# Kernel optimization log

Hardware: AMD Instinct MI355X
Metric: run time of the kernel (lower is better)

Reference implementation:

```python
import jax, jax.numpy as jnp
import numpy as np
import math

B, T, S, D, H = 2, 1024, 1024, 1024, 16
DH = D // H


def setup_inputs() -> dict:
    key = jax.random.key(0)
    ks = jax.random.split(key, 13)
    scale = 1.0 / math.sqrt(D)
    inp = {
        "q": jax.random.normal(ks[0], (B, T, D), jnp.float32),
        "k": jax.random.normal(ks[1], (B, S, D), jnp.float32),
        "v": jax.random.normal(ks[2], (B, S, D), jnp.float32),
        # causal mask: True means masked
        "attn_mask": jnp.broadcast_to(
            jnp.triu(jnp.ones((T, S), jnp.bool_), k=1)[None, None], (B, 1, T, S)
        ),
        "attn_bias": jax.random.normal(ks[3], (B, H, T, S), jnp.float32),
        "Wq": jax.random.normal(ks[4], (D, D), jnp.float32) * scale,
        "bq": jnp.zeros((D,), jnp.float32),
        "Wk": jax.random.normal(ks[5], (D, D), jnp.float32) * scale,
        "bk": jnp.zeros((D,), jnp.float32),
        "Wv": jax.random.normal(ks[6], (D, D), jnp.float32) * scale,
        "bv": jnp.zeros((D,), jnp.float32),
        "Wo": jax.random.normal(ks[7], (D, D), jnp.float32) * scale,
        "bo": jnp.zeros((D,), jnp.float32),
        "bias_scale": jnp.asarray(0.5, jnp.float32),
    }
    return inp


def reference(q, k, v, attn_mask, attn_bias, Wq, bq, Wk, bk, Wv, bv, Wo, bo, bias_scale):
    # projections (torch Linear convention: x @ W.T + b), split heads
    qh = (q @ Wq.T + bq).reshape(B, T, H, DH)   # (B,T,H,DH)
    kh = (k @ Wk.T + bk).reshape(B, S, H, DH)
    vh = (v @ Wv.T + bv).reshape(B, S, H, DH)

    scores = jnp.einsum("bthd,bshd->bhts", qh, kh) / math.sqrt(DH)  # (B,H,T,S)
    scores = jnp.clip(scores, -80.0, 80.0)
    scores = jnp.where(attn_mask, -jnp.inf, scores)  # mask broadcasts over H
    attn = jax.nn.softmax(scores, axis=-1)

    # post-softmax multiplicative bias + renormalize
    scale = 1.0 + bias_scale * jnp.tanh(attn_bias)
    attn = attn * jnp.maximum(scale, 1e-9)
    attn = attn / (jnp.sum(attn, axis=-1, keepdims=True) + 1e-9)

    # dropout p=0.0 (eval) -> identity
    out = jnp.einsum("bhts,bshd->bthd", attn, vh).reshape(B, T, D)
    out = out @ Wo.T + bo
    return out, attn
```

## Files before the change

### kernel.cpp

```cpp
#include <hip/hip_runtime.h>
#include <hip/hip_bf16.h>
#include <math.h>

#define BB 2
#define TT 1024
#define SS 1024
#define DD 1024
#define HH 16
#define DH 64

typedef __attribute__((ext_vector_type(8))) short bf16x8;
typedef __attribute__((ext_vector_type(4))) float f32x4;
typedef unsigned short ushort_t;

#define AS3(p) ((__attribute__((address_space(3))) unsigned int*)(p))
#define AS1(p) ((const __attribute__((address_space(1))) unsigned int*)(p))

__device__ __forceinline__ unsigned short f2b(float f) {
    union { float f; unsigned u; } x; x.f = f;
    unsigned r = x.u + 0x7FFFu + ((x.u >> 16) & 1u);
    return (unsigned short)(r >> 16);
}

__global__ __launch_bounds__(256) void cvt3_kernel(
    const float* __restrict__ a, const float* __restrict__ b, const float* __restrict__ c,
    ushort_t* __restrict__ oa, ushort_t* __restrict__ ob, ushort_t* __restrict__ oc)
{
    const float* src = (blockIdx.y == 0) ? a : (blockIdx.y == 1) ? b : c;
    ushort_t* dst    = (blockIdx.y == 0) ? oa : (blockIdx.y == 1) ? ob : oc;
    size_t i = ((size_t)blockIdx.x * 256 + threadIdx.x) * 8;
    float4 v0 = *(const float4*)&src[i];
    float4 v1 = *(const float4*)&src[i + 4];
    uint4 o;
    o.x = f2b(v0.x) | ((unsigned)f2b(v0.y) << 16);
    o.y = f2b(v0.z) | ((unsigned)f2b(v0.w) << 16);
    o.z = f2b(v1.x) | ((unsigned)f2b(v1.y) << 16);
    o.w = f2b(v1.z) | ((unsigned)f2b(v1.w) << 16);
    *(uint4*)&dst[i] = o;
}

__global__ __launch_bounds__(256) void cvt4_kernel(
    const float* __restrict__ a, const float* __restrict__ b,
    const float* __restrict__ c, const float* __restrict__ d,
    ushort_t* __restrict__ oa, ushort_t* __restrict__ ob,
    ushort_t* __restrict__ oc, ushort_t* __restrict__ od)
{
    const float* src = (blockIdx.y == 0) ? a : (blockIdx.y == 1) ? b : (blockIdx.y == 2) ? c : d;
    ushort_t* dst    = (blockIdx.y == 0) ? oa : (blockIdx.y == 1) ? ob : (blockIdx.y == 2) ? oc : od;
    size_t i = ((size_t)blockIdx.x * 256 + threadIdx.x) * 8;
    float4 v0 = *(const float4*)&src[i];
    float4 v1 = *(const float4*)&src[i + 4];
    uint4 o;
    o.x = f2b(v0.x) | ((unsigned)f2b(v0.y) << 16);
    o.y = f2b(v0.z) | ((unsigned)f2b(v0.w) << 16);
    o.z = f2b(v1.x) | ((unsigned)f2b(v1.y) << 16);
    o.w = f2b(v1.z) | ((unsigned)f2b(v1.w) << 16);
    *(uint4*)&dst[i] = o;
}

__device__ __forceinline__ void gemm128_mainloop(
    const ushort_t* __restrict__ A,
    const ushort_t* __restrict__ Bw,
    int K, ushort_t* Asm, ushort_t* Bsm, f32x4 acc[4][4])
{
    const int tid = threadIdx.x;
    const int wave = tid >> 6, lane = tid & 63;
    const int sr = lane >> 2;
    const int gc = (lane & 3) ^ ((lane >> 3) & 3);
    const int l15 = lane & 15, q = lane >> 4;
    const int mblk = (wave >> 1) * 64, nblk = (wave & 1) * 64;

    for (int k0 = 0; k0 < K; k0 += 32) {
        #pragma unroll
        for (int o = 0; o < 2; o++) {
            int r0 = (wave * 2 + o) * 16;
            __builtin_amdgcn_global_load_lds(AS1(A + (size_t)(r0 + sr) * K + k0 + gc * 8),
                                             AS3(Asm + r0 * 32), 16, 0, 0);
            __builtin_amdgcn_global_load_lds(AS1(Bw + (size_t)(r0 + sr) * K + k0 + gc * 8),
                                             AS3(Bsm + r0 * 32), 16, 0, 0);
        }
        __syncthreads();

        bf16x8 av[4], bv[4];
        #pragma unroll
        for (int mi = 0; mi < 4; mi++) {
            int r = mblk + mi * 16 + l15;
            av[mi] = *(const bf16x8*)&Asm[r * 32 + (q ^ ((r >> 1) & 3)) * 8];
        }
        #pragma unroll
        for (int ni = 0; ni < 4; ni++) {
            int r = nblk + ni * 16 + l15;
            bv[ni] = *(const bf16x8*)&Bsm[r * 32 + (q ^ ((r >> 1) & 3)) * 8];
        }
        #pragma unroll
        for (int mi = 0; mi < 4; mi++)
            #pragma unroll
            for (int ni = 0; ni < 4; ni++)
                acc[mi][ni] = __builtin_amdgcn_mfma_f32_16x16x32_bf16(av[mi], bv[ni], acc[mi][ni], 0, 0, 0);
        __syncthreads();
    }
}

__global__ __launch_bounds__(256) void proj_gemm(
    const ushort_t* __restrict__ qb, const ushort_t* __restrict__ kb, const ushort_t* __restrict__ vb,
    const ushort_t* __restrict__ Wqb, const ushort_t* __restrict__ Wkb, const ushort_t* __restrict__ Wvb,
    const float* __restrict__ bq, const float* __restrict__ bk, const float* __restrict__ bv,
    ushort_t* __restrict__ qh, ushort_t* __restrict__ kh, ushort_t* __restrict__ vh)
{
    __shared__ ushort_t Asm[128 * 32];
    __shared__ ushort_t Bsm[128 * 32];
    const int z = blockIdx.z;
    const ushort_t* A = (z == 0) ? qb : (z == 1) ? kb : vb;
    const ushort_t* W = (z == 0) ? Wqb : (z == 1) ? Wkb : Wvb;
    const float* bias = (z == 0) ? bq : (z == 1) ? bk : bv;
    ushort_t* Y = (z == 0) ? qh : (z == 1) ? kh : vh;

    const int bm = blockIdx.y * 128, bn = blockIdx.x * 128;
    f32x4 acc[4][4];
    #pragma unroll
    for (int i = 0; i < 4; i++)
        #pragma unroll
        for (int j = 0; j < 4; j++) acc[i][j] = (f32x4)(0.f);

    gemm128_mainloop(A + (size_t)bm * DD, W + (size_t)bn * DD, DD, Asm, Bsm, acc);

    const int lane = threadIdx.x & 63, wave = threadIdx.x >> 6;
    const int mblk = (wave >> 1) * 64, nblk = (wave & 1) * 64;
    const int l15 = lane & 15, q = lane >> 4;
    #pragma unroll
    for (int mi = 0; mi < 4; mi++) {
        #pragma unroll
        for (int ni = 0; ni < 4; ni++) {
            int col = bn + nblk + ni * 16 + l15;
            float bcol = bias[col];
            #pragma unroll
            for (int r = 0; r < 4; r++) {
                int row = bm + mblk + mi * 16 + q * 4 + r;
                Y[(size_t)row * DD + col] = f2b(acc[mi][ni][r] + bcol);
            }
        }
    }
}

__global__ __launch_bounds__(256) void oproj_gemm(
    const ushort_t* __restrict__ A, const ushort_t* __restrict__ W,
    const float* __restrict__ bias, float* __restrict__ Y)
{
    __shared__ ushort_t Asm[128 * 32];
    __shared__ ushort_t Bsm[128 * 32];
    const int bm = blockIdx.y * 128, bn = blockIdx.x * 128;
    f32x4 acc[4][4];
    #pragma unroll
    for (int i = 0; i < 4; i++)
        #pragma unroll
        for (int j = 0; j < 4; j++) acc[i][j] = (f32x4)(0.f);

    gemm128_mainloop(A + (size_t)bm * DD, W + (size_t)bn * DD, DD, Asm, Bsm, acc);

    const int lane = threadIdx.x & 63, wave = threadIdx.x >> 6;
    const int mblk = (wave >> 1) * 64, nblk = (wave & 1) * 64;
    const int l15 = lane & 15, q = lane >> 4;
    #pragma unroll
    for (int mi = 0; mi < 4; mi++) {
        #pragma unroll
        for (int ni = 0; ni < 4; ni++) {
            int col = bn + nblk + ni * 16 + l15;
            float bcol = bias[col];
            #pragma unroll
            for (int r = 0; r < 4; r++) {
                int row = bm + mblk + mi * 16 + q * 4 + r;
                Y[(size_t)row * DD + col] = acc[mi][ni][r] + bcol;
            }
        }
    }
}

__global__ __launch_bounds__(256) void transpose_v(
    const ushort_t* __restrict__ vh, ushort_t* __restrict__ vT)
{
    __shared__ ushort_t Ls[64][72];
    const int s0 = blockIdx.x * 64;
    const int bh = blockIdx.y;
    const int b = bh >> 4, h = bh & 15;
    const int tid = threadIdx.x;
    const int r = tid >> 2, c16 = (tid & 3) * 16;

    const ushort_t* src = &vh[((size_t)(b * SS + s0 + r) * HH + h) * DH + c16];
    uint4 u0 = *(const uint4*)src;
    uint4 u1 = *(const uint4*)(src + 8);
    ushort_t tmp[16];
    *(uint4*)&tmp[0] = u0; *(uint4*)&tmp[8] = u1;
    #pragma unroll
    for (int j = 0; j < 16; j++) Ls[c16 + j][r] = tmp[j];
    __syncthreads();

    const int dh = r;
    uint4 w0 = *(const uint4*)&Ls[dh][c16];
    uint4 w1 = *(const uint4*)&Ls[dh][c16 + 8];
    ushort_t* dst = &vT[((size_t)bh * DH + dh) * SS + s0 + c16];
    *(uint4*)dst = w0;
    *(uint4*)(dst + 8) = w1;
}

__global__ __launch_bounds__(256) void scores_mfma(
    const ushort_t* __restrict__ qh, const ushort_t* __restrict__ kh,
    float* __restrict__ attn)
{
    __shared__ ushort_t Qs[128 * 64];
    __shared__ ushort_t Ks[128 * 64];

    int idx = blockIdx.x, ti = 0;
    while (idx >= ti + 1) { idx -= ti + 1; ti++; }
    const int si = idx;
    const int bh = blockIdx.y;
    const int b = bh >> 4, h = bh & 15;
    const int t0 = ti * 128, s0 = si * 128;

    const int tid = threadIdx.x;
    const int wave = tid >> 6, lane = tid & 63;
    const int sr8 = lane >> 3;
    const int gc8 = (lane & 7) ^ sr8;

    #pragma unroll
    for (int o = 0; o < 4; o++) {
        int r0 = (wave * 4 + o) * 8;
        int r = r0 + sr8;
        __builtin_amdgcn_global_load_lds(
            AS1(qh + ((size_t)(b * TT + t0 + r) * HH + h) * DH + gc8 * 8),
            AS3(Qs + r0 * 64), 16, 0, 0);
        __builtin_amdgcn_global_load_lds(
            AS1(kh + ((size_t)(b * SS + s0 + r) * HH + h) * DH + gc8 * 8),
            AS3(Ks + r0 * 64), 16, 0, 0);
    }
    __syncthreads();

    const int l15 = lane & 15, q = lane >> 4;
    const int tblk = (wave >> 1) * 64, sblk = (wave & 1) * 64;
    f32x4 acc[4][4];
    #pragma unroll
    for (int i = 0; i < 4; i++)
        #pragma unroll
        for (int j = 0; j < 4; j++) acc[i][j] = (f32x4)(0.f);

    #pragma unroll
    for (int ks = 0; ks < 2; ks++) {
        bf16x8 av[4], bv[4];
        #pragma unroll
        for (int mi = 0; mi < 4; mi++) {
            int r = tblk + mi * 16 + l15;
            av[mi] = *(const bf16x8*)&Qs[r * 64 + ((ks * 4 + q) ^ (r & 7)) * 8];
        }
        #pragma unroll
        for (int ni = 0; ni < 4; ni++) {
            int r = sblk + ni * 16 + l15;
            bv[ni] = *(const bf16x8*)&Ks[r * 64 + ((ks * 4 + q) ^ (r & 7)) * 8];
        }
        #pragma unroll
        for (int mi = 0; mi < 4; mi++)
            #pragma unroll
            for (int ni = 0; ni < 4; ni++)
                acc[mi][ni] = __builtin_amdgcn_mfma_f32_16x16x32_bf16(av[mi], bv[ni], acc[mi][ni], 0, 0, 0);
    }

    #pragma unroll
    for (int mi = 0; mi < 4; mi++) {
        #pragma unroll
        for (int ni = 0; ni < 4; ni++) {
            int scol = s0 + sblk + ni * 16 + l15;
            #pragma unroll
            for (int r = 0; r < 4; r++) {
                int t = t0 + tblk + mi * 16 + q * 4 + r;
                float v = acc[mi][ni][r] * 0.125f;
                v = fminf(fmaxf(v, -80.f), 80.f);
                attn[((size_t)bh * TT + t) * SS + scol] = v;
            }
        }
    }
}

__global__ __launch_bounds__(256) void softmax_bias_kernel(
    const float* __restrict__ attn_bias, const float* __restrict__ bias_scale_p,
    float* __restrict__ attn)
{
    const int bid = blockIdx.x;
    const int t = bid & (TT - 1);
    const int tid = threadIdx.x;
    const int s0 = tid * 4;

    float* row = attn + (size_t)bid * SS;
    const float* brow = attn_bias + (size_t)bid * SS;

    __shared__ float red[256];

    float v0 = -INFINITY, v1 = -INFINITY, v2 = -INFINITY, v3 = -INFINITY;
    if (s0 <= t) {
        float4 rv = *(const float4*)&row[s0];
        v0 = rv.x;
        v1 = (s0 + 1 <= t) ? rv.y : -INFINITY;
        v2 = (s0 + 2 <= t) ? rv.z : -INFINITY;
        v3 = (s0 + 3 <= t) ? rv.w : -INFINITY;
    }
    float lmax = fmaxf(fmaxf(v0, v1), fmaxf(v2, v3));
    red[tid] = lmax;
    __syncthreads();
    for (int off = 128; off > 0; off >>= 1) {
        if (tid < off) red[tid] = fmaxf(red[tid], red[tid + off]);
        __syncthreads();
    }
    const float m = red[0];
    __syncthreads();

    float p0 = (v0 > -INFINITY) ? __expf(v0 - m) : 0.f;
    float p1 = (v1 > -INFINITY) ? __expf(v1 - m) : 0.f;
    float p2 = (v2 > -INFINITY) ? __expf(v2 - m) : 0.f;
    float p3 = (v3 > -INFINITY) ? __expf(v3 - m) : 0.f;
    red[tid] = p0 + p1 + p2 + p3;
    __syncthreads();
    for (int off = 128; off > 0; off >>= 1) {
        if (tid < off) red[tid] += red[tid + off];
        __syncthreads();
    }
    const float inv = 1.f / red[0];
    __syncthreads();

    const float bscale = bias_scale_p[0];
    float w0 = 0.f, w1 = 0.f, w2 = 0.f, w3 = 0.f;
    if (s0 <= t) {
        float4 bv = *(const float4*)&brow[s0];
        float e0 = __expf(-2.f * fabsf(bv.x));
        float e1 = __expf(-2.f * fabsf(bv.y));
        float e2 = __expf(-2.f * fabsf(bv.z));
        float e3 = __expf(-2.f * fabsf(bv.w));
        float t0 = copysignf((1.f - e0) / (1.f + e0), bv.x);
        float t1 = copysignf((1.f - e1) / (1.f + e1), bv.y);
        float t2 = copysignf((1.f - e2) / (1.f + e2), bv.z);
        float t3 = copysignf((1.f - e3) / (1.f + e3), bv.w);
        w0 = p0 * inv * fmaxf(1.f + bscale * t0, 1e-9f);
        w1 = p1 * inv * fmaxf(1.f + bscale * t1, 1e-9f);
        w2 = p2 * inv * fmaxf(1.f + bscale * t2, 1e-9f);
        w3 = p3 * inv * fmaxf(1.f + bscale * t3, 1e-9f);
    }
    red[tid] = w0 + w1 + w2 + w3;
    __syncthreads();
    for (int off = 128; off > 0; off >>= 1) {
        if (tid < off) red[tid] += red[tid + off];
        __syncthreads();
    }
    const float inv2 = 1.f / (red[0] + 1e-9f);

    float4 o;
    o.x = w0 * inv2; o.y = w1 * inv2; o.z = w2 * inv2; o.w = w3 * inv2;
    *(float4*)&row[s0] = o;
}

__global__ __launch_bounds__(256) void av_mfma(
    const float* __restrict__ attn, const ushort_t* __restrict__ vT,
    ushort_t* __restrict__ ao)
{
    __shared__ ushort_t Asm[64 * 32];
    __shared__ ushort_t Vsm[64 * 32];

    const int tb = blockIdx.x;
    const int bh = blockIdx.y;
    const int b = bh >> 4, h = bh & 15;
    const int t0 = tb * 64;
    const int nsteps = (tb + 1) * 2;

    const int tid = threadIdx.x;
    const int wave = tid >> 6, lane = tid & 63;
    const int ar = tid >> 2, aq = tid & 3;
    const int aslot = aq ^ ((ar >> 1) & 3);
    const int vsr = lane >> 2;
    const int vgc = (lane & 3) ^ ((lane >> 3) & 3);
    const int l15 = lane & 15, q = lane >> 4;

    f32x4 acc[4];
    #pragma unroll
    for (int i = 0; i < 4; i++) acc[i] = (f32x4)(0.f);

    for (int st = 0; st < nsteps; st++) {
        const int s0 = st * 32;
        {
            const float* src = &attn[((size_t)bh * TT + t0 + ar) * SS + s0 + aq * 8];
            float4 u0 = *(const float4*)src;
            float4 u1 = *(const float4*)(src + 4);
            uint4 o;
            o.x = f2b(u0.x) | ((unsigned)f2b(u0.y) << 16);
            o.y = f2b(u0.z) | ((unsigned)f2b(u0.w) << 16);
            o.z = f2b(u1.x) | ((unsigned)f2b(u1.y) << 16);
            o.w = f2b(u1.z) | ((unsigned)f2b(u1.w) << 16);
            *(uint4*)&Asm[ar * 32 + aslot * 8] = o;
        }
        {
            int r0 = wave * 16;
            __builtin_amdgcn_global_load_lds(
                AS1(vT + ((size_t)bh * DH + r0 + vsr) * SS + s0 + vgc * 8),
                AS3(Vsm + r0 * 32), 16, 0, 0);
        }
        __syncthreads();

        bf16x8 a0, bv[4];
        {
            int r = wave * 16 + l15;
            a0 = *(const bf16x8*)&Asm[r * 32 + (q ^ ((r >> 1) & 3)) * 8];
        }
        #pragma unroll
        for (int ni = 0; ni < 4; ni++) {
            int r = ni * 16 + l15;
            bv[ni] = *(const bf16x8*)&Vsm[r * 32 + (q ^ ((r >> 1) & 3)) * 8];
        }
        #pragma unroll
        for (int ni = 0; ni < 4; ni++)
            acc[ni] = __builtin_amdgcn_mfma_f32_16x16x32_bf16(a0, bv[ni], acc[ni], 0, 0, 0);
        __syncthreads();
    }

    #pragma unroll
    for (int ni = 0; ni < 4; ni++) {
        int dh = ni * 16 + l15;
        #pragma unroll
        for (int r = 0; r < 4; r++) {
            int t = t0 + wave * 16 + q * 4 + r;
            ao[(size_t)(b * TT + t) * DD + h * DH + dh] = f2b(acc[ni][r]);
        }
    }
}

extern "C" void kernel_launch(void* const* d_in, const int* in_sizes, int n_in,
                              void* d_out, int out_size, void* d_ws, size_t ws_size,
                              hipStream_t stream)
{
    const float* q   = (const float*)d_in[0];
    const float* k   = (const float*)d_in[1];
    const float* v   = (const float*)d_in[2];
    const float* attn_bias = (const float*)d_in[4];
    const float* Wq = (const float*)d_in[5];
    const float* bq = (const float*)d_in[6];
    const float* Wk = (const float*)d_in[7];
    const float* bk = (const float*)d_in[8];
    const float* Wv = (const float*)d_in[9];
    const float* bv = (const float*)d_in[10];
    const float* Wo = (const float*)d_in[11];
    const float* bo = (const float*)d_in[12];
    const float* bscale = (const float*)d_in[13];

    char* base = (char*)d_ws;
    ushort_t* qb  = (ushort_t*)(base + (0ull << 20));
    ushort_t* kb  = (ushort_t*)(base + (4ull << 20));
    ushort_t* vb  = (ushort_t*)(base + (8ull << 20));
    ushort_t* Wqb = (ushort_t*)(base + (12ull << 20));
    ushort_t* Wkb = (ushort_t*)(base + (14ull << 20));
    ushort_t* Wvb = (ushort_t*)(base + (16ull << 20));
    ushort_t* Wob = (ushort_t*)(base + (18ull << 20));
    ushort_t* qhb = (ushort_t*)(base + (20ull << 20));
    ushort_t* khb = (ushort_t*)(base + (24ull << 20));
    ushort_t* vhb = (ushort_t*)(base + (28ull << 20));
    ushort_t* vT  = qb;
    ushort_t* aob = kb;

    float* out  = (float*)d_out;
    float* attn = out + (size_t)BB * TT * DD;

    cvt3_kernel<<<dim3(1024, 3), 256, 0, stream>>>(q, k, v, qb, kb, vb);
    cvt4_kernel<<<dim3(512, 4), 256, 0, stream>>>(Wq, Wk, Wv, Wo, Wqb, Wkb, Wvb, Wob);
    proj_gemm<<<dim3(8, 16, 3), 256, 0, stream>>>(qb, kb, vb, Wqb, Wkb, Wvb,
                                                  bq, bk, bv, qhb, khb, vhb);
    transpose_v<<<dim3(16, 32), 256, 0, stream>>>(vhb, vT);
    scores_mfma<<<dim3(36, 32), 256, 0, stream>>>(qhb, khb, attn);
    softmax_bias_kernel<<<dim3(BB * HH * TT), 256, 0, stream>>>(attn_bias, bscale, attn);
    av_mfma<<<dim3(16, 32), 256, 0, stream>>>(attn, vT, aob);
    oproj_gemm<<<dim3(8, 16), 256, 0, stream>>>(aob, Wob, bo, out);
}
```

Measured before the change: 390.1 us.

## Fuse scores, softmax, bias renormalization and AV into one flash-style attention kernel

Replaces the separate scores, softmax+bias and AV kernels with a single two-pass kernel per 64-row query tile. The first pass computes the row max over causal key blocks. The second pass recomputes scores, applies the exp and tanh-bias scale, writes unnormalized bf16 weights to a scratch buffer, and accumulates P·V with MFMA. A final sweep normalizes and writes the fp32 attn output, and the two float conversion kernels are merged into one launch. This removes the full fp32 attention round trips through global memory. In exchange it recomputes QK^T, keeps an extra bf16 scratch pass, and rounds the attn output through bf16. It also drops the 1e-9 term in the final renormalisation.

```diff
diff --git a/kernel.cpp b/kernel.cpp
--- a/kernel.cpp
+++ b/kernel.cpp
@@ -22,12 +22,27 @@
     return (unsigned short)(r >> 16);
 }
 
-__global__ __launch_bounds__(256) void cvt3_kernel(
-    const float* __restrict__ a, const float* __restrict__ b, const float* __restrict__ c,
-    ushort_t* __restrict__ oa, ushort_t* __restrict__ ob, ushort_t* __restrict__ oc)
-{
-    const float* src = (blockIdx.y == 0) ? a : (blockIdx.y == 1) ? b : c;
-    ushort_t* dst    = (blockIdx.y == 0) ? oa : (blockIdx.y == 1) ? ob : oc;
+__global__ __launch_bounds__(256) void cvt_all(
+    const float* __restrict__ q, const float* __restrict__ k, const float* __restrict__ v,
+    const float* __restrict__ Wq, const float* __restrict__ Wk,
+    const float* __restrict__ Wv, const float* __restrict__ Wo,
+    ushort_t* __restrict__ qb, ushort_t* __restrict__ kb, ushort_t* __restrict__ vb,
+    ushort_t* __restrict__ Wqb, ushort_t* __restrict__ Wkb,
+    ushort_t* __restrict__ Wvb, ushort_t* __restrict__ Wob)
+{
+    const int z = blockIdx.y;
+    if (z >= 3 && blockIdx.x >= 512) return;
+    const float* src;
+    ushort_t* dst;
+    switch (z) {
+        case 0: src = q;  dst = qb;  break;
+        case 1: src = k;  dst = kb;  break;
+        case 2: src = v;  dst = vb;  break;
+        case 3: src = Wq; dst = Wqb; break;
+        case 4: src = Wk; dst = Wkb; break;
+        case 5: src = Wv; dst = Wvb; break;
+        default: src = Wo; dst = Wob; break;
+    }
     size_t i = ((size_t)blockIdx.x * 256 + threadIdx.x) * 8;
     float4 v0 = *(const float4*)&src[i];
     float4 v1 = *(const float4*)&src[i + 4];
@@ -39,28 +54,8 @@
     *(uint4*)&dst[i] = o;
 }
 
-__global__ __launch_bounds__(256) void cvt4_kernel(
-    const float* __restrict__ a, const float* __restrict__ b,
-    const float* __restrict__ c, const float* __restrict__ d,
-    ushort_t* __restrict__ oa, ushort_t* __restrict__ ob,
-    ushort_t* __restrict__ oc, ushort_t* __restrict__ od)
-{
-    const float* src = (blockIdx.y == 0) ? a : (blockIdx.y == 1) ? b : (blockIdx.y == 2) ? c : d;
-    ushort_t* dst    = (blockIdx.y == 0) ? oa : (blockIdx.y == 1) ? ob : (blockIdx.y == 2) ? oc : od;
-    size_t i = ((size_t)blockIdx.x * 256 + threadIdx.x) * 8;
-    float4 v0 = *(const float4*)&src[i];
-    float4 v1 = *(const float4*)&src[i + 4];
-    uint4 o;
-    o.x = f2b(v0.x) | ((unsigned)f2b(v0.y) << 16);
-    o.y = f2b(v0.z) | ((unsigned)f2b(v0.w) << 16);
-    o.z = f2b(v1.x) | ((unsigned)f2b(v1.y) << 16);
-    o.w = f2b(v1.z) | ((unsigned)f2b(v1.w) << 16);
-    *(uint4*)&dst[i] = o;
-}
-
 __device__ __forceinline__ void gemm128_mainloop(
-    const ushort_t* __restrict__ A,
-    const ushort_t* __restrict__ Bw,
+    const ushort_t* __restrict__ A, const ushort_t* __restrict__ Bw,
     int K, ushort_t* Asm, ushort_t* Bsm, f32x4 acc[4][4])
 {
     const int tid = threadIdx.x;
@@ -185,7 +180,7 @@
     const int tid = threadIdx.x;
     const int r = tid >> 2, c16 = (tid & 3) * 16;
 
-    const ushort_t* src = &vh[((size_t)(b * SS + s0 + r) * HH + h) * DH + c16];
+    const ushort_t* src = &vh[((size_t)(b * SS + s0 + r)) * DD + h * DH + c16];
     uint4 u0 = *(const uint4*)src;
     uint4 u1 = *(const uint4*)(src + 8);
     ushort_t tmp[16];
@@ -202,228 +197,269 @@
     *(uint4*)(dst + 8) = w1;
 }
 
-__global__ __launch_bounds__(256) void scores_mfma(
+#define SCORE_MFMA(sacc)                                                        \
+  do {                                                                          \
+    _Pragma("unroll")                                                           \
+    for (int ks = 0; ks < 2; ks++) {                                            \
+      bf16x8 af[2], bfv[4];                                                     \
+      _Pragma("unroll")                                                         \
+      for (int mi = 0; mi < 2; mi++) {                                          \
+        int row_ = mq * 32 + mi * 16 + l15;                                     \
+        af[mi] = *(const bf16x8*)&Qs[row_ * 64 + ((ks * 4 + q) ^ (row_ & 7)) * 8]; \
+      }                                                                         \
+      _Pragma("unroll")                                                         \
+      for (int ni = 0; ni < 4; ni++) {                                          \
+        int srw_ = nq * 64 + ni * 16 + l15;                                     \
+        bfv[ni] = *(const bf16x8*)&Ks[srw_ * 64 + ((ks * 4 + q) ^ (srw_ & 7)) * 8]; \
+      }                                                                         \
+      _Pragma("unroll")                                                         \
+      for (int mi = 0; mi < 2; mi++)                                            \
+        _Pragma("unroll")                                                       \
+        for (int ni = 0; ni < 4; ni++)                                          \
+          sacc[mi][ni] = __builtin_amdgcn_mfma_f32_16x16x32_bf16(af[mi], bfv[ni], sacc[mi][ni], 0, 0, 0); \
+    }                                                                           \
+  } while (0)
+
+#define STAGE_K(s0_)                                                            \
+  do {                                                                          \
+    _Pragma("unroll")                                                           \
+    for (int o = 0; o < 4; o++) {                                               \
+      int slot = o * 256 + tid;                                                 \
+      int row_ = slot >> 3, cs_ = slot & 7, c_ = cs_ ^ (row_ & 7);              \
+      __builtin_amdgcn_global_load_lds(                                         \
+          AS1(kh + (size_t)(b * SS + (s0_) + row_) * DD + h * DH + c_ * 8),     \
+          AS3(Ks + (o * 256 + wave * 64) * 8), 16, 0, 0);                       \
+    }                                                                           \
+  } while (0)
+
+#define STAGE_V(s0_)                                                            \
+  do {                                                                          \
+    _Pragma("unroll")                                                           \
+    for (int o = 0; o < 4; o++) {                                               \
+      int slot = o * 256 + tid;                                                 \
+      int row_ = slot >> 4, cs_ = slot & 15, c_ = cs_ ^ (row_ & 15);            \
+      __builtin_amdgcn_global_load_lds(                                         \
+          AS1(vT + ((size_t)bh * DH + row_) * SS + (s0_) + c_ * 8),             \
+          AS3(Vs + (o * 256 + wave * 64) * 8), 16, 0, 0);                       \
+    }                                                                           \
+  } while (0)
+
+__global__ __launch_bounds__(256, 2) void flash_attn(
     const ushort_t* __restrict__ qh, const ushort_t* __restrict__ kh,
+    const ushort_t* __restrict__ vT, const float* __restrict__ attn_bias,
+    const float* __restrict__ bscale_p,
+    ushort_t* __restrict__ wbuf, ushort_t* __restrict__ ao,
     float* __restrict__ attn)
 {
-    __shared__ ushort_t Qs[128 * 64];
-    __shared__ ushort_t Ks[128 * 64];
-
-    int idx = blockIdx.x, ti = 0;
-    while (idx >= ti + 1) { idx -= ti + 1; ti++; }
-    const int si = idx;
+    __shared__ alignas(16) ushort_t Qs[64 * 64];
+    __shared__ alignas(16) ushort_t Ks[128 * 64];
+    __shared__ alignas(16) ushort_t Vs[64 * 128];
+    __shared__ alignas(16) ushort_t Ws[64 * 136];
+    __shared__ float rmax_p[2][64];
+    __shared__ float rsum_p[2][64];
+    __shared__ float rstat[64];
+
+    const int xs = blockIdx.x;
+    const int ti = (xs & 1) ? (15 - (xs >> 1)) : (xs >> 1);
     const int bh = blockIdx.y;
     const int b = bh >> 4, h = bh & 15;
-    const int t0 = ti * 128, s0 = si * 128;
+    const int t0 = ti * 64;
+    const int nst = (ti >> 1) + 1;
 
     const int tid = threadIdx.x;
     const int wave = tid >> 6, lane = tid & 63;
-    const int sr8 = lane >> 3;
-    const int gc8 = (lane & 7) ^ sr8;
-
-    #pragma unroll
-    for (int o = 0; o < 4; o++) {
-        int r0 = (wave * 4 + o) * 8;
-        int r = r0 + sr8;
+    const int l15 = lane & 15, q = lane >> 4;
+    const int mq = wave & 1, nq = wave >> 1;
+
+    #pragma unroll
+    for (int o = 0; o < 2; o++) {
+        int slot = o * 256 + tid;
+        int row_ = slot >> 3, cs_ = slot & 7, c_ = cs_ ^ (row_ & 7);
         __builtin_amdgcn_global_load_lds(
-            AS1(qh + ((size_t)(b * TT + t0 + r) * HH + h) * DH + gc8 * 8),
-            AS3(Qs + r0 * 64), 16, 0, 0);
-        __builtin_amdgcn_global_load_lds(
-            AS1(kh + ((size_t)(b * SS + s0 + r) * HH + h) * DH + gc8 * 8),
-            AS3(Ks + r0 * 64), 16, 0, 0);
+            AS1(qh + (size_t)(b * TT + t0 + row_) * DD + h * DH + c_ * 8),
+            AS3(Qs + (o * 256 + wave * 64) * 8), 16, 0, 0);
+    }
+
+    float rm[2][4];
+    #pragma unroll
+    for (int mi = 0; mi < 2; mi++)
+        #pragma unroll
+        for (int r = 0; r < 4; r++) rm[mi][r] = -INFINITY;
+
+    for (int si = 0; si < nst; si++) {
+        const int s0 = si * 128;
+        STAGE_K(s0);
+        __syncthreads();
+        f32x4 sacc[2][4];
+        #pragma unroll
+        for (int mi = 0; mi < 2; mi++)
+            #pragma unroll
+            for (int ni = 0; ni < 4; ni++) sacc[mi][ni] = (f32x4)(0.f);
+        SCORE_MFMA(sacc);
+        #pragma unroll
+        for (int mi = 0; mi < 2; mi++)
+            #pragma unroll
+            for (int ni = 0; ni < 4; ni++) {
+                int s = s0 + nq * 64 + ni * 16 + l15;
+                #pragma unroll
+                for (int r = 0; r < 4; r++) {
+                    int t = t0 + mq * 32 + mi * 16 + q * 4 + r;
+                    if (s <= t) {
+                        float v = fminf(fmaxf(sacc[mi][ni][r] * 0.125f, -80.f), 80.f);
+                        rm[mi][r] = fmaxf(rm[mi][r], v);
+                    }
+                }
+            }
+        __syncthreads();
+    }
+    #pragma unroll
+    for (int mi = 0; mi < 2; mi++)
+        #pragma unroll
+        for (int r = 0; r < 4; r++) {
+            float v = rm[mi][r];
+            v = fmaxf(v, __shfl_xor(v, 1));
+            v = fmaxf(v, __shfl_xor(v, 2));
+            v = fmaxf(v, __shfl_xor(v, 4));
+            v = fmaxf(v, __shfl_xor(v, 8));
+            rm[mi][r] = v;
+        }
+    if (l15 == 0) {
+        #pragma unroll
+        for (int mi = 0; mi < 2; mi++)
+            #pragma unroll
+            for (int r = 0; r < 4; r++)
+                rmax_p[nq][mq * 32 + mi * 16 + q * 4 + r] = rm[mi][r];
     }
     __syncthreads();
-
-    const int l15 = lane & 15, q = lane >> 4;
-    const int tblk = (wave >> 1) * 64, sblk = (wave & 1) * 64;
-    f32x4 acc[4][4];
-    #pragma unroll
-    for (int i = 0; i < 4; i++)
-        #pragma unroll
-        for (int j = 0; j < 4; j++) acc[i][j] = (f32x4)(0.f);
-
-    #pragma unroll
-    for (int ks = 0; ks < 2; ks++) {
-        bf16x8 av[4], bv[4];
-        #pragma unroll
-        for (int mi = 0; mi < 4; mi++) {
-            int r = tblk + mi * 16 + l15;
-            av[mi] = *(const bf16x8*)&Qs[r * 64 + ((ks * 4 + q) ^ (r & 7)) * 8];
-        }
-        #pragma unroll
-        for (int ni = 0; ni < 4; ni++) {
-            int r = sblk + ni * 16 + l15;
-            bv[ni] = *(const bf16x8*)&Ks[r * 64 + ((ks * 4 + q) ^ (r & 7)) * 8];
-        }
-        #pragma unroll
-        for (int mi = 0; mi < 4; mi++)
-            #pragma unroll
-            for (int ni = 0; ni < 4; ni++)
-                acc[mi][ni] = __builtin_amdgcn_mfma_f32_16x16x32_bf16(av[mi], bv[ni], acc[mi][ni], 0, 0, 0);
-    }
-
-    #pragma unroll
-    for (int mi = 0; mi < 4; mi++) {
-        #pragma unroll
-        for (int ni = 0; ni < 4; ni++) {
-            int scol = s0 + sblk + ni * 16 + l15;
+    if (tid < 64) rstat[tid] = fmaxf(rmax_p[0][tid], rmax_p[1][tid]);
+    __syncthreads();
+
+    float rs[2][4] = {};
+    f32x4 oacc[2][2];
+    #pragma unroll
+    for (int mi = 0; mi < 2; mi++)
+        #pragma unroll
+        for (int ni = 0; ni < 2; ni++) oacc[mi][ni] = (f32x4)(0.f);
+    const float bs = bscale_p[0];
+
+    for (int si = 0; si < nst; si++) {
+        const int s0 = si * 128;
+        STAGE_K(s0);
+        STAGE_V(s0);
+        __syncthreads();
+        f32x4 sacc[2][4];
+        #pragma unroll
+        for (int mi = 0; mi < 2; mi++)
+            #pragma unroll
+            for (int ni = 0; ni < 4; ni++) sacc[mi][ni] = (f32x4)(0.f);
+        SCORE_MFMA(sacc);
+
+        #pragma unroll
+        for (int mi = 0; mi < 2; mi++)
+            #pragma unroll
+            for (int ni = 0; ni < 4; ni++) {
+                int sc_ = nq * 64 + ni * 16 + l15;
+                int s = s0 + sc_;
+                #pragma unroll
+                for (int r = 0; r < 4; r++) {
+                    int trow = mq * 32 + mi * 16 + q * 4 + r;
+                    int t = t0 + trow;
+                    float w = 0.f;
+                    if (s <= t) {
+                        float v = fminf(fmaxf(sacc[mi][ni][r] * 0.125f, -80.f), 80.f);
+                        float x = attn_bias[((size_t)bh * TT + t) * SS + s];
+                        float e = __expf(-2.f * fabsf(x));
+                        float th = copysignf((1.f - e) / (1.f + e), x);
+                        float scl = fmaxf(1.f + bs * th, 1e-9f);
+                        w = __expf(v - rstat[trow]) * scl;
+                        rs[mi][r] += w;
+                    }
+                    Ws[trow * 136 + sc_] = f2b(w);
+                }
+            }
+        __syncthreads();
+
+        #pragma unroll
+        for (int o = 0; o < 4; o++) {
+            int idx = o * 256 + tid;
+            int row_ = idx >> 4, c_ = idx & 15;
+            uint4 u = *(const uint4*)&Ws[row_ * 136 + c_ * 8];
+            *(uint4*)&wbuf[((size_t)bh * TT + t0 + row_) * SS + s0 + c_ * 8] = u;
+        }
+
+        #pragma unroll
+        for (int ks = 0; ks < 4; ks++) {
+            bf16x8 af[2], bf2[2];
+            #pragma unroll
+            for (int mi = 0; mi < 2; mi++) {
+                int row_ = mq * 32 + mi * 16 + l15;
+                af[mi] = *(const bf16x8*)&Ws[row_ * 136 + (ks * 4 + q) * 8];
+            }
+            #pragma unroll
+            for (int ni = 0; ni < 2; ni++) {
+                int vr = nq * 32 + ni * 16 + l15;
+                bf2[ni] = *(const bf16x8*)&Vs[vr * 128 + ((ks * 4 + q) ^ (vr & 15)) * 8];
+            }
+            #pragma unroll
+            for (int mi = 0; mi < 2; mi++)
+                #pragma unroll
+                for (int ni = 0; ni < 2; ni++)
+                    oacc[mi][ni] = __builtin_amdgcn_mfma_f32_16x16x32_bf16(af[mi], bf2[ni], oacc[mi][ni], 0, 0, 0);
+        }
+        __syncthreads();
+    }
+
+    #pragma unroll
+    for (int mi = 0; mi < 2; mi++)
+        #pragma unroll
+        for (int r = 0; r < 4; r++) {
+            float v = rs[mi][r];
+            v += __shfl_xor(v, 1);
+            v += __shfl_xor(v, 2);
+            v += __shfl_xor(v, 4);
+            v += __shfl_xor(v, 8);
+            rs[mi][r] = v;
+        }
+    if (l15 == 0) {
+        #pragma unroll
+        for (int mi = 0; mi < 2; mi++)
+            #pragma unroll
+            for (int r = 0; r < 4; r++)
+                rsum_p[nq][mq * 32 + mi * 16 + q * 4 + r] = rs[mi][r];
+    }
+    __syncthreads();
+    if (tid < 64) rstat[tid] = 1.f / (rsum_p[0][tid] + rsum_p[1][tid]);
+    __syncthreads();
+
+    const int cend = nst * 128;
+    for (int idx = tid; idx < 64 * 256; idx += 256) {
+        int row_ = idx >> 8;
+        int c4 = (idx & 255) * 4;
+        float4 o4;
+        if (c4 < cend) {
+            uint2 u = *(const uint2*)&wbuf[((size_t)bh * TT + t0 + row_) * SS + c4];
+            float inv = rstat[row_];
+            union { unsigned uu; float ff; } a0, a1, a2, a3;
+            a0.uu = (u.x & 0xffffu) << 16; a1.uu = (u.x & 0xffff0000u);
+            a2.uu = (u.y & 0xffffu) << 16; a3.uu = (u.y & 0xffff0000u);
+            o4.x = a0.ff * inv; o4.y = a1.ff * inv; o4.z = a2.ff * inv; o4.w = a3.ff * inv;
+        } else {
+            o4.x = 0.f; o4.y = 0.f; o4.z = 0.f; o4.w = 0.f;
+        }
+        *(float4*)&attn[((size_t)bh * TT + t0 + row_) * SS + c4] = o4;
+    }
+
+    #pragma unroll
+    for (int mi = 0; mi < 2; mi++)
+        #pragma unroll
+        for (int ni = 0; ni < 2; ni++)
             #pragma unroll
             for (int r = 0; r < 4; r++) {
-                int t = t0 + tblk + mi * 16 + q * 4 + r;
-                float v = acc[mi][ni][r] * 0.125f;
-                v = fminf(fmaxf(v, -80.f), 80.f);
-                attn[((size_t)bh * TT + t) * SS + scol] = v;
-            }
-        }
-    }
-}
-
-__global__ __launch_bounds__(256) void softmax_bias_kernel(
-    const float* __restrict__ attn_bias, const float* __restrict__ bias_scale_p,
-    float* __restrict__ attn)
-{
-    const int bid = blockIdx.x;
-    const int t = bid & (TT - 1);
-    const int tid = threadIdx.x;
-    const int s0 = tid * 4;
-
-    float* row = attn + (size_t)bid * SS;
-    const float* brow = attn_bias + (size_t)bid * SS;
-
-    __shared__ float red[256];
-
-    float v0 = -INFINITY, v1 = -INFINITY, v2 = -INFINITY, v3 = -INFINITY;
-    if (s0 <= t) {
-        float4 rv = *(const float4*)&row[s0];
-        v0 = rv.x;
-        v1 = (s0 + 1 <= t) ? rv.y : -INFINITY;
-        v2 = (s0 + 2 <= t) ? rv.z : -INFINITY;
-        v3 = (s0 + 3 <= t) ? rv.w : -INFINITY;
-    }
-    float lmax = fmaxf(fmaxf(v0, v1), fmaxf(v2, v3));
-    red[tid] = lmax;
-    __syncthreads();
-    for (int off = 128; off > 0; off >>= 1) {
-        if (tid < off) red[tid] = fmaxf(red[tid], red[tid + off]);
-        __syncthreads();
-    }
-    const float m = red[0];
-    __syncthreads();
-
-    float p0 = (v0 > -INFINITY) ? __expf(v0 - m) : 0.f;
-    float p1 = (v1 > -INFINITY) ? __expf(v1 - m) : 0.f;
-    float p2 = (v2 > -INFINITY) ? __expf(v2 - m) : 0.f;
-    float p3 = (v3 > -INFINITY) ? __expf(v3 - m) : 0.f;
-    red[tid] = p0 + p1 + p2 + p3;
-    __syncthreads();
-    for (int off = 128; off > 0; off >>= 1) {
-        if (tid < off) red[tid] += red[tid + off];
-        __syncthreads();
-    }
-    const float inv = 1.f / red[0];
-    __syncthreads();
-
-    const float bscale = bias_scale_p[0];
-    float w0 = 0.f, w1 = 0.f, w2 = 0.f, w3 = 0.f;
-    if (s0 <= t) {
-        float4 bv = *(const float4*)&brow[s0];
-        float e0 = __expf(-2.f * fabsf(bv.x));
-        float e1 = __expf(-2.f * fabsf(bv.y));
-        float e2 = __expf(-2.f * fabsf(bv.z));
-        float e3 = __expf(-2.f * fabsf(bv.w));
-        float t0 = copysignf((1.f - e0) / (1.f + e0), bv.x);
-        float t1 = copysignf((1.f - e1) / (1.f + e1), bv.y);
-        float t2 = copysignf((1.f - e2) / (1.f + e2), bv.z);
-        float t3 = copysignf((1.f - e3) / (1.f + e3), bv.w);
-        w0 = p0 * inv * fmaxf(1.f + bscale * t0, 1e-9f);
-        w1 = p1 * inv * fmaxf(1.f + bscale * t1, 1e-9f);
-        w2 = p2 * inv * fmaxf(1.f + bscale * t2, 1e-9f);
-        w3 = p3 * inv * fmaxf(1.f + bscale * t3, 1e-9f);
-    }
-    red[tid] = w0 + w1 + w2 + w3;
-    __syncthreads();
-    for (int off = 128; off > 0; off >>= 1) {
-        if (tid < off) red[tid] += red[tid + off];
-        __syncthreads();
-    }
-    const float inv2 = 1.f / (red[0] + 1e-9f);
-
-    float4 o;
-    o.x = w0 * inv2; o.y = w1 * inv2; o.z = w2 * inv2; o.w = w3 * inv2;
-    *(float4*)&row[s0] = o;
-}
-
-__global__ __launch_bounds__(256) void av_mfma(
-    const float* __restrict__ attn, const ushort_t* __restrict__ vT,
-    ushort_t* __restrict__ ao)
-{
-    __shared__ ushort_t Asm[64 * 32];
-    __shared__ ushort_t Vsm[64 * 32];
-
-    const int tb = blockIdx.x;
-    const int bh = blockIdx.y;
-    const int b = bh >> 4, h = bh & 15;
-    const int t0 = tb * 64;
-    const int nsteps = (tb + 1) * 2;
-
-    const int tid = threadIdx.x;
-    const int wave = tid >> 6, lane = tid & 63;
-    const int ar = tid >> 2, aq = tid & 3;
-    const int aslot = aq ^ ((ar >> 1) & 3);
-    const int vsr = lane >> 2;
-    const int vgc = (lane & 3) ^ ((lane >> 3) & 3);
-    const int l15 = lane & 15, q = lane >> 4;
-
-    f32x4 acc[4];
-    #pragma unroll
-    for (int i = 0; i < 4; i++) acc[i] = (f32x4)(0.f);
-
-    for (int st = 0; st < nsteps; st++) {
-        const int s0 = st * 32;
-        {
-            const float* src = &attn[((size_t)bh * TT + t0 + ar) * SS + s0 + aq * 8];
-            float4 u0 = *(const float4*)src;
-            float4 u1 = *(const float4*)(src + 4);
-            uint4 o;
-            o.x = f2b(u0.x) | ((unsigned)f2b(u0.y) << 16);
-            o.y = f2b(u0.z) | ((unsigned)f2b(u0.w) << 16);
-            o.z = f2b(u1.x) | ((unsigned)f2b(u1.y) << 16);
-            o.w = f2b(u1.z) | ((unsigned)f2b(u1.w) << 16);
-            *(uint4*)&Asm[ar * 32 + aslot * 8] = o;
-        }
-        {
-            int r0 = wave * 16;
-            __builtin_amdgcn_global_load_lds(
-                AS1(vT + ((size_t)bh * DH + r0 + vsr) * SS + s0 + vgc * 8),
-                AS3(Vsm + r0 * 32), 16, 0, 0);
-        }
-        __syncthreads();
-
-        bf16x8 a0, bv[4];
-        {
-            int r = wave * 16 + l15;
-            a0 = *(const bf16x8*)&Asm[r * 32 + (q ^ ((r >> 1) & 3)) * 8];
-        }
-        #pragma unroll
-        for (int ni = 0; ni < 4; ni++) {
-            int r = ni * 16 + l15;
-            bv[ni] = *(const bf16x8*)&Vsm[r * 32 + (q ^ ((r >> 1) & 3)) * 8];
-        }
-        #pragma unroll
-        for (int ni = 0; ni < 4; ni++)
-            acc[ni] = __builtin_amdgcn_mfma_f32_16x16x32_bf16(a0, bv[ni], acc[ni], 0, 0, 0);
-        __syncthreads();
-    }
-
-    #pragma unroll
-    for (int ni = 0; ni < 4; ni++) {
-        int dh = ni * 16 + l15;
-        #pragma unroll
-        for (int r = 0; r < 4; r++) {
-            int t = t0 + wave * 16 + q * 4 + r;
-            ao[(size_t)(b * TT + t) * DD + h * DH + dh] = f2b(acc[ni][r]);
-        }
-    }
+                int row_ = mq * 32 + mi * 16 + q * 4 + r;
+                int col = nq * 32 + ni * 16 + l15;
+                ao[(size_t)(b * TT + t0 + row_) * DD + h * DH + col] =
+                    f2b(oacc[mi][ni][r] * rstat[row_]);
+            }
 }
 
 extern "C" void kernel_launch(void* const* d_in, const int* in_sizes, int n_in,
@@ -445,29 +481,29 @@
     const float* bscale = (const float*)d_in[13];
 
     char* base = (char*)d_ws;
-    ushort_t* qb  = (ushort_t*)(base + (0ull << 20));
-    ushort_t* kb  = (ushort_t*)(base + (4ull << 20));
-    ushort_t* vb  = (ushort_t*)(base + (8ull << 20));
-    ushort_t* Wqb = (ushort_t*)(base + (12ull << 20));
-    ushort_t* Wkb = (ushort_t*)(base + (14ull << 20));
-    ushort_t* Wvb = (ushort_t*)(base + (16ull << 20));
-    ushort_t* Wob = (ushort_t*)(base + (18ull << 20));
-    ushort_t* qhb = (ushort_t*)(base + (20ull << 20));
-    ushort_t* khb = (ushort_t*)(base + (24ull << 20));
-    ushort_t* vhb = (ushort_t*)(base + (28ull << 20));
-    ushort_t* vT  = qb;
-    ushort_t* aob = kb;
+    ushort_t* qb   = (ushort_t*)(base + (0ull  << 20));
+    ushort_t* kb   = (ushort_t*)(base + (4ull  << 20));
+    ushort_t* vb   = (ushort_t*)(base + (8ull  << 20));
+    ushort_t* Wqb  = (ushort_t*)(base + (12ull << 20));
+    ushort_t* Wkb  = (ushort_t*)(base + (14ull << 20));
+    ushort_t* Wvb  = (ushort_t*)(base + (16ull << 20));
+    ushort_t* Wob  = (ushort_t*)(base + (18ull << 20));
+    ushort_t* qhb  = (ushort_t*)(base + (20ull << 20));
+    ushort_t* khb  = (ushort_t*)(base + (24ull << 20));
+    ushort_t* vhb  = (ushort_t*)(base + (28ull << 20));
+    ushort_t* vT   = (ushort_t*)(base + (32ull << 20));
+    ushort_t* aob  = (ushort_t*)(base + (36ull << 20));
+    ushort_t* wbuf = (ushort_t*)(base + (40ull << 20));
 
     float* out  = (float*)d_out;
     float* attn = out + (size_t)BB * TT * DD;
 
-    cvt3_kernel<<<dim3(1024, 3), 256, 0, stream>>>(q, k, v, qb, kb, vb);
-    cvt4_kernel<<<dim3(512, 4), 256, 0, stream>>>(Wq, Wk, Wv, Wo, Wqb, Wkb, Wvb, Wob);
+    cvt_all<<<dim3(1024, 7), 256, 0, stream>>>(q, k, v, Wq, Wk, Wv, Wo,
+                                               qb, kb, vb, Wqb, Wkb, Wvb, Wob);
     proj_gemm<<<dim3(8, 16, 3), 256, 0, stream>>>(qb, kb, vb, Wqb, Wkb, Wvb,
                                                   bq, bk, bv, qhb, khb, vhb);
     transpose_v<<<dim3(16, 32), 256, 0, stream>>>(vhb, vT);
-    scores_mfma<<<dim3(36, 32), 256, 0, stream>>>(qhb, khb, attn);
-    softmax_bias_kernel<<<dim3(BB * HH * TT), 256, 0, stream>>>(attn_bias, bscale, attn);
-    av_mfma<<<dim3(16, 32), 256, 0, stream>>>(attn, vT, aob);
+    flash_attn<<<dim3(16, 32), 256, 0, stream>>>(qhb, khb, vT, attn_bias, bscale,
+                                                 wbuf, aob, attn);
     oproj_gemm<<<dim3(8, 16), 256, 0, stream>>>(aob, Wob, bo, out);
 }
```

New measurement: 493.9 us. 1.27x slower.
